# Performance work log

Hardware: AMD Instinct MI355X
Metric: run time of the kernel (lower is better)

## Reference

```python
import jax, jax.numpy as jnp
import numpy as np

N = 50000
H = 256
EPS = 1e-5

def setup_inputs() -> dict:
    key = jax.random.key(0)
    ks = jax.random.split(key, 8)
    d = 128
    inp = {
        'x': jax.random.normal(ks[0], (N, d), jnp.float32),
        'edge_index': jax.random.randint(ks[1], (2, 800000), 0, N, jnp.int64),
        'W1': jax.random.normal(ks[2], (d, H), jnp.float32) * (2.0 / d) ** 0.5,
        'b1': jnp.zeros((H,), jnp.float32),
        'g1': jnp.ones((H,), jnp.float32),
        'be1': jnp.zeros((H,), jnp.float32),
        'W2': jax.random.normal(ks[3], (H, H), jnp.float32) * (2.0 / H) ** 0.5,
        'b2': jnp.zeros((H,), jnp.float32),
        'g2': jnp.ones((H,), jnp.float32),
        'be2': jnp.zeros((H,), jnp.float32),
        'W3': jax.random.normal(ks[4], (H, H), jnp.float32) * (2.0 / H) ** 0.5,
        'b3': jnp.zeros((H,), jnp.float32),
        'g3': jnp.ones((H,), jnp.float32),
        'be3': jnp.zeros((H,), jnp.float32),
        'Wf1': jax.random.normal(ks[5], (H, H // 2), jnp.float32) * (2.0 / H) ** 0.5,
        'bf1': jnp.zeros((H // 2,), jnp.float32),
        'Wf2': jax.random.normal(ks[6], (H // 2, 1), jnp.float32) * (2.0 / (H // 2)) ** 0.5,
        'bf2': jnp.zeros((1,), jnp.float32),
    }
    return inp

def _gcn_norm(edge_index):
    # add self-loops, symmetric normalization (PyG GCNConv defaults)
    loop = jnp.arange(N, dtype=edge_index.dtype)
    row = jnp.concatenate([edge_index[0], loop])  # source
    col = jnp.concatenate([edge_index[1], loop])  # target
    deg = jax.ops.segment_sum(jnp.ones_like(col, jnp.float32), col, num_segments=N)
    dis = jnp.where(deg > 0, jax.lax.rsqrt(deg), 0.0)
    norm = dis[row] * dis[col]  # [E+N]
    return row, col, norm

def _conv(x, W, b, row, col, norm):
    xw = x @ W                       # [N,H]
    msg = xw[row] * norm[:, None]    # gather + scale, [E+N,H]
    out = jax.ops.segment_sum(msg, col, num_segments=N)
    return out + b

def _ln(x, g, b):
    mu = jnp.mean(x, axis=-1, keepdims=True)
    var = jnp.var(x, axis=-1, keepdims=True)
    return (x - mu) * jax.lax.rsqrt(var + EPS) * g + b

def reference(x, edge_index, W1, b1, g1, be1, W2, b2, g2, be2, W3, b3, g3, be3, Wf1, bf1, Wf2, bf2):
    row, col, norm = _gcn_norm(edge_index)
    x1 = jax.nn.relu(_ln(_conv(x, W1, b1, row, col, norm), g1, be1))
    x2 = jax.nn.relu(_ln(_conv(x1, W2, b2, row, col, norm), g2, be2)) + 0.7 * x1
    x3 = jax.nn.relu(_ln(_conv(x2, W3, b3, row, col, norm), g3, be3)) * 0.7 + x2
    h = jax.nn.relu(x3 @ Wf1 + bf1)
    return h @ Wf2 + bf2  # [N,1]
```

## Files before the change

kernel.cpp:

```cpp
#include <hip/hip_runtime.h>
#include <cstdint>
#include <cstddef>

#define HDIM 256
#define DIN 128
#define EPSV 1e-5f
#define SCHUNK 1024

typedef __attribute__((ext_vector_type(8))) short short8;
typedef __attribute__((ext_vector_type(4))) float f32x4;

__device__ __forceinline__ float bf2f(unsigned int u16) {
  union { unsigned int i; float f; } v; v.i = u16 << 16; return v.f;
}
__device__ __forceinline__ unsigned short f2bf(float f) {
  union { float f; unsigned int i; } v; v.f = f;
  unsigned int u = v.i;
  return (unsigned short)((u + 0x7fffu + ((u >> 16) & 1u)) >> 16);
}
__device__ __forceinline__ float4 ldbf4(const unsigned short* p) {
  uint2 v = *(const uint2*)p;
  return make_float4(bf2f(v.x & 0xffffu), bf2f(v.x >> 16),
                     bf2f(v.y & 0xffffu), bf2f(v.y >> 16));
}
__device__ __forceinline__ void stbf4(unsigned short* p, float a, float b, float c, float d) {
  uint2 o;
  o.x = (unsigned int)f2bf(a) | ((unsigned int)f2bf(b) << 16);
  o.y = (unsigned int)f2bf(c) | ((unsigned int)f2bf(d) << 16);
  *(uint2*)p = o;
}

__global__ __launch_bounds__(256) void zero_i_k(int* deg, int* cur, int n) {
  int i = blockIdx.x * 256 + threadIdx.x;
  if (i < n) { deg[i] = 0; cur[i] = 0; }
}

__global__ __launch_bounds__(256) void hist_k(const int* __restrict__ col, int* deg, int e) {
  int i = blockIdx.x * 256 + threadIdx.x;
  if (i < e) atomicAdd(&deg[col[i]], 1);
}

__global__ __launch_bounds__(256) void scanA_k(const int* __restrict__ deg,
                                               int* __restrict__ row_ptr,
                                               int* __restrict__ blockSums,
                                               float* __restrict__ dis, int n) {
  __shared__ int waveSums[4];
  const int tid = threadIdx.x, lane = tid & 63, w = tid >> 6;
  const int base = blockIdx.x * SCHUNK + tid * 4;
  int v0 = 0, v1 = 0, v2 = 0, v3 = 0;
  if (base + 0 < n) v0 = deg[base + 0];
  if (base + 1 < n) v1 = deg[base + 1];
  if (base + 2 < n) v2 = deg[base + 2];
  if (base + 3 < n) v3 = deg[base + 3];
  if (base + 0 < n) dis[base + 0] = rsqrtf((float)(v0 + 1));
  if (base + 1 < n) dis[base + 1] = rsqrtf((float)(v1 + 1));
  if (base + 2 < n) dis[base + 2] = rsqrtf((float)(v2 + 1));
  if (base + 3 < n) dis[base + 3] = rsqrtf((float)(v3 + 1));
  int tsum = v0 + v1 + v2 + v3;
  int inc = tsum;
#pragma unroll
  for (int off = 1; off < 64; off <<= 1) {
    int t = __shfl_up(inc, off);
    if (lane >= off) inc += t;
  }
  if (lane == 63) waveSums[w] = inc;
  __syncthreads();
  int woff = 0;
#pragma unroll
  for (int k = 0; k < 4; ++k) woff += (k < w) ? waveSums[k] : 0;
  int excl = woff + inc - tsum;
  if (base + 0 < n) row_ptr[base + 0] = excl;
  if (base + 1 < n) row_ptr[base + 1] = excl + v0;
  if (base + 2 < n) row_ptr[base + 2] = excl + v0 + v1;
  if (base + 3 < n) row_ptr[base + 3] = excl + v0 + v1 + v2;
  if (tid == 255) blockSums[blockIdx.x] = woff + inc;
}

__global__ __launch_bounds__(256) void scanB_k(int* blockSums, int nb) {
  __shared__ int waveSums[4];
  const int tid = threadIdx.x, lane = tid & 63, w = tid >> 6;
  int v = (tid < nb) ? blockSums[tid] : 0;
  int inc = v;
#pragma unroll
  for (int off = 1; off < 64; off <<= 1) {
    int t = __shfl_up(inc, off);
    if (lane >= off) inc += t;
  }
  if (lane == 63) waveSums[w] = inc;
  __syncthreads();
  int woff = 0;
#pragma unroll
  for (int k = 0; k < 4; ++k) woff += (k < w) ? waveSums[k] : 0;
  if (tid < nb) blockSums[tid] = woff + inc - v;
}

__global__ __launch_bounds__(256) void scanC_k(int* __restrict__ row_ptr,
                                               const int* __restrict__ blockSums,
                                               int n, int e) {
  const int base = blockIdx.x * SCHUNK + threadIdx.x * 4;
  const int add = blockSums[blockIdx.x];
#pragma unroll
  for (int k = 0; k < 4; ++k)
    if (base + k < n) row_ptr[base + k] += add;
  if (blockIdx.x == 0 && threadIdx.x == 0) row_ptr[n] = e;
}

__global__ __launch_bounds__(256) void fill_k(const int* __restrict__ row,
                                              const int* __restrict__ col,
                                              const int* __restrict__ row_ptr,
                                              int* cur, int* srcs, int e) {
  int i = blockIdx.x * 256 + threadIdx.x;
  if (i < e) {
    int c = col[i];
    int p = row_ptr[c] + atomicAdd(&cur[c], 1);
    srcs[p] = row[i];
  }
}

__device__ __forceinline__ void packW(const float* __restrict__ W,
                                      unsigned short* __restrict__ out,
                                      int idx, int C) {
  int j = idx & 7, lane = (idx >> 3) & 63, rest = idx >> 9;
  int NSUB = C >> 4;
  int ns = rest % NSUB, kb = rest / NSUB;
  int k = kb * 32 + (lane >> 4) * 8 + j;
  int c = ns * 16 + (lane & 15);
  out[idx] = f2bf(W[(size_t)k * C + c]);
}

__global__ __launch_bounds__(256) void prep_k(
    const float* __restrict__ W1, const float* __restrict__ W2,
    const float* __restrict__ W3, const float* __restrict__ Wf1,
    const float* __restrict__ x,
    unsigned short* __restrict__ W1p, unsigned short* __restrict__ W2p,
    unsigned short* __restrict__ W3p, unsigned short* __restrict__ Wf1p,
    unsigned short* __restrict__ xbf, int nx) {
  int idx = blockIdx.x * 256 + threadIdx.x;
  const int s0 = DIN * HDIM, s1 = s0 + HDIM * HDIM, s2 = s1 + HDIM * HDIM,
            s3 = s2 + HDIM * 128;
  if (idx < s0) packW(W1, W1p, idx, HDIM);
  else if (idx < s1) packW(W2, W2p, idx - s0, HDIM);
  else if (idx < s2) packW(W3, W3p, idx - s1, HDIM);
  else if (idx < s3) packW(Wf1, Wf1p, idx - s2, 128);
  else if (idx - s3 < nx) xbf[idx - s3] = f2bf(x[idx - s3]);
}

__global__ __launch_bounds__(256) void gather256_k(
    const unsigned short* __restrict__ x, const int* __restrict__ row_ptr,
    const int* __restrict__ srcs, const float* __restrict__ dis,
    unsigned short* __restrict__ out, int n) {
  int i = blockIdx.x * 4 + (threadIdx.x >> 6);
  int lane = threadIdx.x & 63;
  if (i >= n) return;
  int beg = row_ptr[i], end = row_ptr[i + 1];
  const int co = lane * 4;
  float di = dis[i];
  float4 sv = ldbf4(x + (size_t)i * 256 + co);
  float4 acc = make_float4(di * sv.x, di * sv.y, di * sv.z, di * sv.w);
  int j = beg;
  for (; j + 8 <= end; j += 8) {
    int r0 = srcs[j], r1 = srcs[j + 1], r2 = srcs[j + 2], r3 = srcs[j + 3];
    int r4 = srcs[j + 4], r5 = srcs[j + 5], r6 = srcs[j + 6], r7 = srcs[j + 7];
    float d0 = dis[r0], d1 = dis[r1], d2 = dis[r2], d3 = dis[r3];
    float d4 = dis[r4], d5 = dis[r5], d6 = dis[r6], d7 = dis[r7];
    float4 v0 = ldbf4(x + (size_t)r0 * 256 + co);
    float4 v1 = ldbf4(x + (size_t)r1 * 256 + co);
    float4 v2 = ldbf4(x + (size_t)r2 * 256 + co);
    float4 v3 = ldbf4(x + (size_t)r3 * 256 + co);
    float4 v4 = ldbf4(x + (size_t)r4 * 256 + co);
    float4 v5 = ldbf4(x + (size_t)r5 * 256 + co);
    float4 v6 = ldbf4(x + (size_t)r6 * 256 + co);
    float4 v7 = ldbf4(x + (size_t)r7 * 256 + co);
    acc.x += ((d0*v0.x + d1*v1.x) + (d2*v2.x + d3*v3.x)) + ((d4*v4.x + d5*v5.x) + (d6*v6.x + d7*v7.x));
    acc.y += ((d0*v0.y + d1*v1.y) + (d2*v2.y + d3*v3.y)) + ((d4*v4.y + d5*v5.y) + (d6*v6.y + d7*v7.y));
    acc.z += ((d0*v0.z + d1*v1.z) + (d2*v2.z + d3*v3.z)) + ((d4*v4.z + d5*v5.z) + (d6*v6.z + d7*v7.z));
    acc.w += ((d0*v0.w + d1*v1.w) + (d2*v2.w + d3*v3.w)) + ((d4*v4.w + d5*v5.w) + (d6*v6.w + d7*v7.w));
  }
  for (; j < end; ++j) {
    int r = srcs[j];
    float d = dis[r];
    float4 v = ldbf4(x + (size_t)r * 256 + co);
    acc.x += d * v.x; acc.y += d * v.y; acc.z += d * v.z; acc.w += d * v.w;
  }
  stbf4(out + (size_t)i * 256 + co, di * acc.x, di * acc.y, di * acc.z, di * acc.w);
}

__global__ __launch_bounds__(256) void gather128_k(
    const unsigned short* __restrict__ x, const int* __restrict__ row_ptr,
    const int* __restrict__ srcs, const float* __restrict__ dis,
    unsigned short* __restrict__ out, int n) {
  int i = blockIdx.x * 4 + (threadIdx.x >> 6);
  int lane = threadIdx.x & 63;
  if (i >= n) return;
  int beg = row_ptr[i], end = row_ptr[i + 1];
  const int co = lane * 2;
  float di = dis[i];
  unsigned int sv = *(const unsigned int*)(x + (size_t)i * 128 + co);
  float ax = di * bf2f(sv & 0xffffu), ay = di * bf2f(sv >> 16);
  int j = beg;
  for (; j + 8 <= end; j += 8) {
    int r0 = srcs[j], r1 = srcs[j + 1], r2 = srcs[j + 2], r3 = srcs[j + 3];
    int r4 = srcs[j + 4], r5 = srcs[j + 5], r6 = srcs[j + 6], r7 = srcs[j + 7];
    float d0 = dis[r0], d1 = dis[r1], d2 = dis[r2], d3 = dis[r3];
    float d4 = dis[r4], d5 = dis[r5], d6 = dis[r6], d7 = dis[r7];
    unsigned int u0 = *(const unsigned int*)(x + (size_t)r0 * 128 + co);
    unsigned int u1 = *(const unsigned int*)(x + (size_t)r1 * 128 + co);
    unsigned int u2 = *(const unsigned int*)(x + (size_t)r2 * 128 + co);
    unsigned int u3 = *(const unsigned int*)(x + (size_t)r3 * 128 + co);
    unsigned int u4 = *(const unsigned int*)(x + (size_t)r4 * 128 + co);
    unsigned int u5 = *(const unsigned int*)(x + (size_t)r5 * 128 + co);
    unsigned int u6 = *(const unsigned int*)(x + (size_t)r6 * 128 + co);
    unsigned int u7 = *(const unsigned int*)(x + (size_t)r7 * 128 + co);
    ax += ((d0*bf2f(u0&0xffffu) + d1*bf2f(u1&0xffffu)) + (d2*bf2f(u2&0xffffu) + d3*bf2f(u3&0xffffu)))
        + ((d4*bf2f(u4&0xffffu) + d5*bf2f(u5&0xffffu)) + (d6*bf2f(u6&0xffffu) + d7*bf2f(u7&0xffffu)));
    ay += ((d0*bf2f(u0>>16) + d1*bf2f(u1>>16)) + (d2*bf2f(u2>>16) + d3*bf2f(u3>>16)))
        + ((d4*bf2f(u4>>16) + d5*bf2f(u5>>16)) + (d6*bf2f(u6>>16) + d7*bf2f(u7>>16)));
  }
  for (; j < end; ++j) {
    int r = srcs[j];
    float d = dis[r];
    unsigned int u = *(const unsigned int*)(x + (size_t)r * 128 + co);
    ax += d * bf2f(u & 0xffffu);
    ay += d * bf2f(u >> 16);
  }
  unsigned int o = (unsigned int)f2bf(di * ax) | ((unsigned int)f2bf(di * ay) << 16);
  *(unsigned int*)(out + (size_t)i * 128 + co) = o;
}

template<int MODE, int K>
__global__ __launch_bounds__(512) void gemmln_k(
    const unsigned short* __restrict__ A, const unsigned short* __restrict__ Wp,
    const float* __restrict__ bias, const float* __restrict__ gam,
    const float* __restrict__ bet, const unsigned short* __restrict__ xprev,
    unsigned short* __restrict__ out, int n) {
  constexpr int CN = 256, NSUB = 16, KC = K / 32;
  __shared__ float red_s[64][4], red_q[64][4];
  const int t = threadIdx.x;
  const int w = t >> 6, lane = t & 63;
  const int rg = w & 1, cg = w >> 1;
  const int gq = lane >> 4, i = lane & 15;
  const int m0 = blockIdx.x * 64;
  const int r0 = m0 + rg * 32 + i, r1 = r0 + 16;
  const int l0 = r0 < n ? r0 : n - 1, l1 = r1 < n ? r1 : n - 1;
  const unsigned short* a0 = A + (size_t)l0 * K + gq * 8;
  const unsigned short* a1 = A + (size_t)l1 * K + gq * 8;
  const short8* wp = (const short8*)Wp + (size_t)(cg * 4) * 64 + lane;

  f32x4 acc[2][4];
#pragma unroll
  for (int rr = 0; rr < 2; ++rr)
#pragma unroll
    for (int j = 0; j < 4; ++j) acc[rr][j] = (f32x4){0.f, 0.f, 0.f, 0.f};

  short8 af0 = *(const short8*)a0;
  short8 af1 = *(const short8*)a1;
  short8 wf[4];
#pragma unroll
  for (int j = 0; j < 4; ++j) wf[j] = wp[j * 64];

#pragma unroll
  for (int kc = 0; kc < KC; ++kc) {
    short8 naf0, naf1, nwf[4];
    if (kc + 1 < KC) {
      naf0 = *(const short8*)(a0 + (kc + 1) * 32);
      naf1 = *(const short8*)(a1 + (kc + 1) * 32);
#pragma unroll
      for (int j = 0; j < 4; ++j) nwf[j] = wp[(size_t)(kc + 1) * NSUB * 64 + j * 64];
    }
#pragma unroll
    for (int j = 0; j < 4; ++j) {
      acc[0][j] = __builtin_amdgcn_mfma_f32_16x16x32_bf16(wf[j], af0, acc[0][j], 0, 0, 0);
      acc[1][j] = __builtin_amdgcn_mfma_f32_16x16x32_bf16(wf[j], af1, acc[1][j], 0, 0, 0);
    }
    if (kc + 1 < KC) {
      af0 = naf0; af1 = naf1;
#pragma unroll
      for (int j = 0; j < 4; ++j) wf[j] = nwf[j];
    }
  }

  const int colb = cg * 64 + gq * 4;
  float s0 = 0.f, q0 = 0.f, s1 = 0.f, q1 = 0.f;
#pragma unroll
  for (int j = 0; j < 4; ++j) {
    f32x4 b4 = *(const f32x4*)(bias + colb + j * 16);
#pragma unroll
    for (int r = 0; r < 4; ++r) {
      acc[0][j][r] += b4[r];
      acc[1][j][r] += b4[r];
      float v = acc[0][j][r]; s0 += v; q0 += v * v;
      float u = acc[1][j][r]; s1 += u; q1 += u * u;
    }
  }
  s0 += __shfl_xor(s0, 16); s0 += __shfl_xor(s0, 32);
  q0 += __shfl_xor(q0, 16); q0 += __shfl_xor(q0, 32);
  s1 += __shfl_xor(s1, 16); s1 += __shfl_xor(s1, 32);
  q1 += __shfl_xor(q1, 16); q1 += __shfl_xor(q1, 32);
  if (gq == 0) {
    red_s[rg * 32 + i][cg] = s0;      red_q[rg * 32 + i][cg] = q0;
    red_s[rg * 32 + 16 + i][cg] = s1; red_q[rg * 32 + 16 + i][cg] = q1;
  }
  __syncthreads();

#pragma unroll
  for (int rr = 0; rr < 2; ++rr) {
    int il = rg * 32 + rr * 16 + i;
    int r = m0 + il;
    if (r >= n) continue;
    float ss = (red_s[il][0] + red_s[il][1]) + (red_s[il][2] + red_s[il][3]);
    float qq = (red_q[il][0] + red_q[il][1]) + (red_q[il][2] + red_q[il][3]);
    float mu = ss * (1.f / CN);
    float inv = rsqrtf(qq * (1.f / CN) - mu * mu + EPSV);
    unsigned short* op = out + (size_t)r * CN + colb;
    const unsigned short* pp = (MODE != 0) ? (xprev + (size_t)r * CN + colb) : nullptr;
#pragma unroll
    for (int j = 0; j < 4; ++j) {
      f32x4 g4 = *(const f32x4*)(gam + colb + j * 16);
      f32x4 e4 = *(const f32x4*)(bet + colb + j * 16);
      float o0 = fmaxf((acc[rr][j][0] - mu) * inv * g4[0] + e4[0], 0.f);
      float o1 = fmaxf((acc[rr][j][1] - mu) * inv * g4[1] + e4[1], 0.f);
      float o2 = fmaxf((acc[rr][j][2] - mu) * inv * g4[2] + e4[2], 0.f);
      float o3 = fmaxf((acc[rr][j][3] - mu) * inv * g4[3] + e4[3], 0.f);
      if (MODE == 1) {
        float4 pv = ldbf4(pp + j * 16);
        o0 += 0.7f * pv.x; o1 += 0.7f * pv.y; o2 += 0.7f * pv.z; o3 += 0.7f * pv.w;
      } else if (MODE == 2) {
        float4 pv = ldbf4(pp + j * 16);
        o0 = o0 * 0.7f + pv.x; o1 = o1 * 0.7f + pv.y;
        o2 = o2 * 0.7f + pv.z; o3 = o3 * 0.7f + pv.w;
      }
      stbf4(op + j * 16, o0, o1, o2, o3);
    }
  }
}

__global__ __launch_bounds__(256) void gemmdot_k(
    const unsigned short* __restrict__ A, const unsigned short* __restrict__ Wp,
    const float* __restrict__ b1, const float* __restrict__ w2,
    const float* __restrict__ b2, float* __restrict__ out, int n) {
  constexpr int K = 256, NSUB = 8, KC = 8;
  __shared__ float redh[64][2];
  const int t = threadIdx.x;
  const int w = t >> 6, lane = t & 63;
  const int rg = w & 1, cg = w >> 1;
  const int gq = lane >> 4, i = lane & 15;
  const int m0 = blockIdx.x * 64;
  const int r0 = m0 + rg * 32 + i, r1 = r0 + 16;
  const int l0 = r0 < n ? r0 : n - 1, l1 = r1 < n ? r1 : n - 1;
  const unsigned short* a0 = A + (size_t)l0 * K + gq * 8;
  const unsigned short* a1 = A + (size_t)l1 * K + gq * 8;
  const short8* wp = (const short8*)Wp + (size_t)(cg * 4) * 64 + lane;

  f32x4 acc[2][4];
#pragma unroll
  for (int rr = 0; rr < 2; ++rr)
#pragma unroll
    for (int j = 0; j < 4; ++j) acc[rr][j] = (f32x4){0.f, 0.f, 0.f, 0.f};

  short8 af0 = *(const short8*)a0;
  short8 af1 = *(const short8*)a1;
  short8 wf[4];
#pragma unroll
  for (int j = 0; j < 4; ++j) wf[j] = wp[j * 64];

#pragma unroll
  for (int kc = 0; kc < KC; ++kc) {
    short8 naf0, naf1, nwf[4];
    if (kc + 1 < KC) {
      naf0 = *(const short8*)(a0 + (kc + 1) * 32);
      naf1 = *(const short8*)(a1 + (kc + 1) * 32);
#pragma unroll
      for (int j = 0; j < 4; ++j) nwf[j] = wp[(size_t)(kc + 1) * NSUB * 64 + j * 64];
    }
#pragma unroll
    for (int j = 0; j < 4; ++j) {
      acc[0][j] = __builtin_amdgcn_mfma_f32_16x16x32_bf16(wf[j], af0, acc[0][j], 0, 0, 0);
      acc[1][j] = __builtin_amdgcn_mfma_f32_16x16x32_bf16(wf[j], af1, acc[1][j], 0, 0, 0);
    }
    if (kc + 1 < KC) {
      af0 = naf0; af1 = naf1;
#pragma unroll
      for (int j = 0; j < 4; ++j) wf[j] = nwf[j];
    }
  }

  const int colb = cg * 64 + gq * 4;
  float p0 = 0.f, p1 = 0.f;
#pragma unroll
  for (int j = 0; j < 4; ++j) {
    f32x4 bb = *(const f32x4*)(b1 + colb + j * 16);
    f32x4 ww = *(const f32x4*)(w2 + colb + j * 16);
#pragma unroll
    for (int r = 0; r < 4; ++r) {
      p0 += fmaxf(acc[0][j][r] + bb[r], 0.f) * ww[r];
      p1 += fmaxf(acc[1][j][r] + bb[r], 0.f) * ww[r];
    }
  }
  p0 += __shfl_xor(p0, 16); p0 += __shfl_xor(p0, 32);
  p1 += __shfl_xor(p1, 16); p1 += __shfl_xor(p1, 32);
  if (gq == 0) {
    redh[rg * 32 + i][cg] = p0;
    redh[rg * 32 + 16 + i][cg] = p1;
  }
  __syncthreads();
  if (t < 64) {
    int r = m0 + t;
    if (r < n) out[r] = redh[t][0] + redh[t][1] + b2[0];
  }
}

extern "C" void kernel_launch(void* const* d_in, const int* in_sizes, int n_in,
                              void* d_out, int out_size, void* d_ws, size_t ws_size,
                              hipStream_t stream) {
  const float* x   = (const float*)d_in[0];
  const int*   ei  = (const int*)d_in[1];
  const float* W1  = (const float*)d_in[2];
  const float* b1  = (const float*)d_in[3];
  const float* g1  = (const float*)d_in[4];
  const float* be1 = (const float*)d_in[5];
  const float* W2  = (const float*)d_in[6];
  const float* b2  = (const float*)d_in[7];
  const float* g2  = (const float*)d_in[8];
  const float* be2 = (const float*)d_in[9];
  const float* W3  = (const float*)d_in[10];
  const float* b3  = (const float*)d_in[11];
  const float* g3  = (const float*)d_in[12];
  const float* be3 = (const float*)d_in[13];
  const float* Wf1 = (const float*)d_in[14];
  const float* bf1 = (const float*)d_in[15];
  const float* Wf2 = (const float*)d_in[16];
  const float* bf2 = (const float*)d_in[17];
  float* out = (float*)d_out;

  const int n = in_sizes[0] / DIN;
  const int e = in_sizes[1] / 2;
  const int* row = ei;
  const int* col = ei + e;

  char* ws = (char*)d_ws;
  size_t off = 0;
  auto alloc = [&](size_t bytes) -> void* {
    void* p = ws + off;
    off = (off + bytes + 255) & ~(size_t)255;
    return p;
  };
  float*          dis     = (float*)alloc((size_t)n * 4);
  int*            deg_i   = (int*)alloc((size_t)n * 4);
  int*            cur     = (int*)alloc((size_t)n * 4);
  int*            row_ptr = (int*)alloc((size_t)(n + 1) * 4);
  int*            bsums   = (int*)alloc((size_t)256 * 4);
  int*            srcs    = (int*)alloc((size_t)e * 4);
  unsigned short* W1p     = (unsigned short*)alloc((size_t)DIN * HDIM * 2);
  unsigned short* W2p     = (unsigned short*)alloc((size_t)HDIM * HDIM * 2);
  unsigned short* W3p     = (unsigned short*)alloc((size_t)HDIM * HDIM * 2);
  unsigned short* Wf1p    = (unsigned short*)alloc((size_t)HDIM * 128 * 2);
  unsigned short* xbf     = (unsigned short*)alloc((size_t)n * DIN * 2);
  unsigned short* agg     = (unsigned short*)alloc((size_t)n * HDIM * 2);
  unsigned short* x1      = (unsigned short*)alloc((size_t)n * HDIM * 2);
  unsigned short* x2      = (unsigned short*)alloc((size_t)n * HDIM * 2);
  unsigned short* a1      = agg;
  unsigned short* x3      = x1;

  const int nb  = (n + 255) / 256;
  const int eb  = (e + 255) / 256;
  const int lnb = (n + 3) / 4;
  const int gb  = (n + 63) / 64;
  const int sb_ = (n + SCHUNK - 1) / SCHUNK;
  const int prep_tot = DIN * HDIM + HDIM * HDIM + HDIM * HDIM + HDIM * 128 + n * DIN;

  zero_i_k<<<nb, 256, 0, stream>>>(deg_i, cur, n);
  hist_k<<<eb, 256, 0, stream>>>(col, deg_i, e);
  scanA_k<<<sb_, 256, 0, stream>>>(deg_i, row_ptr, bsums, dis, n);
  scanB_k<<<1, 256, 0, stream>>>(bsums, sb_);
  scanC_k<<<sb_, 256, 0, stream>>>(row_ptr, bsums, n, e);
  fill_k<<<eb, 256, 0, stream>>>(row, col, row_ptr, cur, srcs, e);

  prep_k<<<(prep_tot + 255) / 256, 256, 0, stream>>>(W1, W2, W3, Wf1, x,
                                                     W1p, W2p, W3p, Wf1p, xbf, n * DIN);

  gather128_k<<<lnb, 256, 0, stream>>>(xbf, row_ptr, srcs, dis, a1, n);
  gemmln_k<0, DIN><<<gb, 512, 0, stream>>>(a1, W1p, b1, g1, be1, nullptr, x1, n);

  gather256_k<<<lnb, 256, 0, stream>>>(x1, row_ptr, srcs, dis, agg, n);
  gemmln_k<1, HDIM><<<gb, 512, 0, stream>>>(agg, W2p, b2, g2, be2, x1, x2, n);

  gather256_k<<<lnb, 256, 0, stream>>>(x2, row_ptr, srcs, dis, agg, n);
  gemmln_k<2, HDIM><<<gb, 512, 0, stream>>>(agg, W3p, b3, g3, be3, x2, x3, n);

  gemmdot_k<<<gb, 256, 0, stream>>>(x3, Wf1p, bf1, Wf2, bf2, out, n);
}
```

Measured before the change: 470.6 us.

## Prescale gather sources by inverse sqrt degree and widen gather loads to 16 bytes

```diff
diff --git a/kernel.cpp b/kernel.cpp
--- a/kernel.cpp
+++ b/kernel.cpp
@@ -29,6 +29,11 @@
   o.y = (unsigned int)f2bf(c) | ((unsigned int)f2bf(d) << 16);
   *(uint2*)p = o;
 }
+#define ACC8(u) do { \
+    acc[0] += bf2f((u).x & 0xffffu); acc[1] += bf2f((u).x >> 16); \
+    acc[2] += bf2f((u).y & 0xffffu); acc[3] += bf2f((u).y >> 16); \
+    acc[4] += bf2f((u).z & 0xffffu); acc[5] += bf2f((u).z >> 16); \
+    acc[6] += bf2f((u).w & 0xffffu); acc[7] += bf2f((u).w >> 16); } while (0)
 
 __global__ __launch_bounds__(256) void zero_i_k(int* deg, int* cur, int n) {
   int i = blockIdx.x * 256 + threadIdx.x;
@@ -131,10 +136,10 @@
 __global__ __launch_bounds__(256) void prep_k(
     const float* __restrict__ W1, const float* __restrict__ W2,
     const float* __restrict__ W3, const float* __restrict__ Wf1,
-    const float* __restrict__ x,
+    const float* __restrict__ x, const float* __restrict__ dis,
     unsigned short* __restrict__ W1p, unsigned short* __restrict__ W2p,
     unsigned short* __restrict__ W3p, unsigned short* __restrict__ Wf1p,
-    unsigned short* __restrict__ xbf, int nx) {
+    unsigned short* __restrict__ xs, int nx) {
   int idx = blockIdx.x * 256 + threadIdx.x;
   const int s0 = DIN * HDIM, s1 = s0 + HDIM * HDIM, s2 = s1 + HDIM * HDIM,
             s3 = s2 + HDIM * 128;
@@ -142,89 +147,118 @@
   else if (idx < s1) packW(W2, W2p, idx - s0, HDIM);
   else if (idx < s2) packW(W3, W3p, idx - s1, HDIM);
   else if (idx < s3) packW(Wf1, Wf1p, idx - s2, 128);
-  else if (idx - s3 < nx) xbf[idx - s3] = f2bf(x[idx - s3]);
+  else {
+    int o = idx - s3;
+    if (o < nx) xs[o] = f2bf(x[o] * dis[o >> 7]);
+  }
 }
 
 __global__ __launch_bounds__(256) void gather256_k(
-    const unsigned short* __restrict__ x, const int* __restrict__ row_ptr,
+    const unsigned short* __restrict__ xs, const int* __restrict__ row_ptr,
     const int* __restrict__ srcs, const float* __restrict__ dis,
     unsigned short* __restrict__ out, int n) {
-  int i = blockIdx.x * 4 + (threadIdx.x >> 6);
+  int wv = blockIdx.x * 4 + (threadIdx.x >> 6);
   int lane = threadIdx.x & 63;
-  if (i >= n) return;
-  int beg = row_ptr[i], end = row_ptr[i + 1];
-  const int co = lane * 4;
-  float di = dis[i];
-  float4 sv = ldbf4(x + (size_t)i * 256 + co);
-  float4 acc = make_float4(di * sv.x, di * sv.y, di * sv.z, di * sv.w);
+  int half = lane >> 5, li = lane & 31;
+  int i = wv * 2 + half;
+  bool valid = i < n;
+  int ic = valid ? i : n - 1;
+  int beg = row_ptr[ic], end = row_ptr[ic + 1];
+  float di = dis[ic];
+  const int co = li * 8;
+  const unsigned short* xb = xs + co;
+  float acc[8];
+  {
+    uint4 v = *(const uint4*)(xb + (size_t)ic * 256);
+    acc[0] = bf2f(v.x & 0xffffu); acc[1] = bf2f(v.x >> 16);
+    acc[2] = bf2f(v.y & 0xffffu); acc[3] = bf2f(v.y >> 16);
+    acc[4] = bf2f(v.z & 0xffffu); acc[5] = bf2f(v.z >> 16);
+    acc[6] = bf2f(v.w & 0xffffu); acc[7] = bf2f(v.w >> 16);
+  }
   int j = beg;
-  for (; j + 8 <= end; j += 8) {
-    int r0 = srcs[j], r1 = srcs[j + 1], r2 = srcs[j + 2], r3 = srcs[j + 3];
-    int r4 = srcs[j + 4], r5 = srcs[j + 5], r6 = srcs[j + 6], r7 = srcs[j + 7];
-    float d0 = dis[r0], d1 = dis[r1], d2 = dis[r2], d3 = dis[r3];
-    float d4 = dis[r4], d5 = dis[r5], d6 = dis[r6], d7 = dis[r7];
-    float4 v0 = ldbf4(x + (size_t)r0 * 256 + co);
-    float4 v1 = ldbf4(x + (size_t)r1 * 256 + co);
-    float4 v2 = ldbf4(x + (size_t)r2 * 256 + co);
-    float4 v3 = ldbf4(x + (size_t)r3 * 256 + co);
-    float4 v4 = ldbf4(x + (size_t)r4 * 256 + co);
-    float4 v5 = ldbf4(x + (size_t)r5 * 256 + co);
-    float4 v6 = ldbf4(x + (size_t)r6 * 256 + co);
-    float4 v7 = ldbf4(x + (size_t)r7 * 256 + co);
-    acc.x += ((d0*v0.x + d1*v1.x) + (d2*v2.x + d3*v3.x)) + ((d4*v4.x + d5*v5.x) + (d6*v6.x + d7*v7.x));
-    acc.y += ((d0*v0.y + d1*v1.y) + (d2*v2.y + d3*v3.y)) + ((d4*v4.y + d5*v5.y) + (d6*v6.y + d7*v7.y));
-    acc.z += ((d0*v0.z + d1*v1.z) + (d2*v2.z + d3*v3.z)) + ((d4*v4.z + d5*v5.z) + (d6*v6.z + d7*v7.z));
-    acc.w += ((d0*v0.w + d1*v1.w) + (d2*v2.w + d3*v3.w)) + ((d4*v4.w + d5*v5.w) + (d6*v6.w + d7*v7.w));
+  int4 sA, sB;
+  if (j + 8 <= end) { sA = *(const int4*)(srcs + j); sB = *(const int4*)(srcs + j + 4); }
+  for (; j + 8 <= end;) {
+    int4 cA = sA, cB = sB;
+    j += 8;
+    if (j + 8 <= end) { sA = *(const int4*)(srcs + j); sB = *(const int4*)(srcs + j + 4); }
+    uint4 u0 = *(const uint4*)(xb + (size_t)cA.x * 256);
+    uint4 u1 = *(const uint4*)(xb + (size_t)cA.y * 256);
+    uint4 u2 = *(const uint4*)(xb + (size_t)cA.z * 256);
+    uint4 u3 = *(const uint4*)(xb + (size_t)cA.w * 256);
+    uint4 u4 = *(const uint4*)(xb + (size_t)cB.x * 256);
+    uint4 u5 = *(const uint4*)(xb + (size_t)cB.y * 256);
+    uint4 u6 = *(const uint4*)(xb + (size_t)cB.z * 256);
+    uint4 u7 = *(const uint4*)(xb + (size_t)cB.w * 256);
+    ACC8(u0); ACC8(u1); ACC8(u2); ACC8(u3);
+    ACC8(u4); ACC8(u5); ACC8(u6); ACC8(u7);
   }
   for (; j < end; ++j) {
-    int r = srcs[j];
-    float d = dis[r];
-    float4 v = ldbf4(x + (size_t)r * 256 + co);
-    acc.x += d * v.x; acc.y += d * v.y; acc.z += d * v.z; acc.w += d * v.w;
-  }
-  stbf4(out + (size_t)i * 256 + co, di * acc.x, di * acc.y, di * acc.z, di * acc.w);
+    uint4 u = *(const uint4*)(xb + (size_t)srcs[j] * 256);
+    ACC8(u);
+  }
+  if (valid) {
+    uint4 o;
+    o.x = (unsigned int)f2bf(di * acc[0]) | ((unsigned int)f2bf(di * acc[1]) << 16);
+    o.y = (unsigned int)f2bf(di * acc[2]) | ((unsigned int)f2bf(di * acc[3]) << 16);
+    o.z = (unsigned int)f2bf(di * acc[4]) | ((unsigned int)f2bf(di * acc[5]) << 16);
+    o.w = (unsigned int)f2bf(di * acc[6]) | ((unsigned int)f2bf(di * acc[7]) << 16);
+    *(uint4*)(out + (size_t)i * 256 + co) = o;
+  }
 }
 
 __global__ __launch_bounds__(256) void gather128_k(
-    const unsigned short* __restrict__ x, const int* __restrict__ row_ptr,
+    const unsigned short* __restrict__ xs, const int* __restrict__ row_ptr,
     const int* __restrict__ srcs, const float* __restrict__ dis,
     unsigned short* __restrict__ out, int n) {
-  int i = blockIdx.x * 4 + (threadIdx.x >> 6);
+  int wv = blockIdx.x * 4 + (threadIdx.x >> 6);
   int lane = threadIdx.x & 63;
-  if (i >= n) return;
-  int beg = row_ptr[i], end = row_ptr[i + 1];
-  const int co = lane * 2;
-  float di = dis[i];
-  unsigned int sv = *(const unsigned int*)(x + (size_t)i * 128 + co);
-  float ax = di * bf2f(sv & 0xffffu), ay = di * bf2f(sv >> 16);
+  int q = lane >> 4, li = lane & 15;
+  int i = wv * 4 + q;
+  bool valid = i < n;
+  int ic = valid ? i : n - 1;
+  int beg = row_ptr[ic], end = row_ptr[ic + 1];
+  float di = dis[ic];
+  const int co = li * 8;
+  const unsigned short* xb = xs + co;
+  float acc[8];
+  {
+    uint4 v = *(const uint4*)(xb + (size_t)ic * 128);
+    acc[0] = bf2f(v.x & 0xffffu); acc[1] = bf2f(v.x >> 16);
+    acc[2] = bf2f(v.y & 0xffffu); acc[3] = bf2f(v.y >> 16);
+    acc[4] = bf2f(v.z & 0xffffu); acc[5] = bf2f(v.z >> 16);
+    acc[6] = bf2f(v.w & 0xffffu); acc[7] = bf2f(v.w >> 16);
+  }
   int j = beg;
-  for (; j + 8 <= end; j += 8) {
-    int r0 = srcs[j], r1 = srcs[j + 1], r2 = srcs[j + 2], r3 = srcs[j + 3];
-    int r4 = srcs[j + 4], r5 = srcs[j + 5], r6 = srcs[j + 6], r7 = srcs[j + 7];
-    float d0 = dis[r0], d1 = dis[r1], d2 = dis[r2], d3 = dis[r3];
-    float d4 = dis[r4], d5 = dis[r5], d6 = dis[r6], d7 = dis[r7];
-    unsigned int u0 = *(const unsigned int*)(x + (size_t)r0 * 128 + co);
-    unsigned int u1 = *(const unsigned int*)(x + (size_t)r1 * 128 + co);
-    unsigned int u2 = *(const unsigned int*)(x + (size_t)r2 * 128 + co);
-    unsigned int u3 = *(const unsigned int*)(x + (size_t)r3 * 128 + co);
-    unsigned int u4 = *(const unsigned int*)(x + (size_t)r4 * 128 + co);
-    unsigned int u5 = *(const unsigned int*)(x + (size_t)r5 * 128 + co);
-    unsigned int u6 = *(const unsigned int*)(x + (size_t)r6 * 128 + co);
-    unsigned int u7 = *(const unsigned int*)(x + (size_t)r7 * 128 + co);
-    ax += ((d0*bf2f(u0&0xffffu) + d1*bf2f(u1&0xffffu)) + (d2*bf2f(u2&0xffffu) + d3*bf2f(u3&0xffffu)))
-        + ((d4*bf2f(u4&0xffffu) + d5*bf2f(u5&0xffffu)) + (d6*bf2f(u6&0xffffu) + d7*bf2f(u7&0xffffu)));
-    ay += ((d0*bf2f(u0>>16) + d1*bf2f(u1>>16)) + (d2*bf2f(u2>>16) + d3*bf2f(u3>>16)))
-        + ((d4*bf2f(u4>>16) + d5*bf2f(u5>>16)) + (d6*bf2f(u6>>16) + d7*bf2f(u7>>16)));
+  int4 sA, sB;
+  if (j + 8 <= end) { sA = *(const int4*)(srcs + j); sB = *(const int4*)(srcs + j + 4); }
+  for (; j + 8 <= end;) {
+    int4 cA = sA, cB = sB;
+    j += 8;
+    if (j + 8 <= end) { sA = *(const int4*)(srcs + j); sB = *(const int4*)(srcs + j + 4); }
+    uint4 u0 = *(const uint4*)(xb + (size_t)cA.x * 128);
+    uint4 u1 = *(const uint4*)(xb + (size_t)cA.y * 128);
+    uint4 u2 = *(const uint4*)(xb + (size_t)cA.z * 128);
+    uint4 u3 = *(const uint4*)(xb + (size_t)cA.w * 128);
+    uint4 u4 = *(const uint4*)(xb + (size_t)cB.x * 128);
+    uint4 u5 = *(const uint4*)(xb + (size_t)cB.y * 128);
+    uint4 u6 = *(const uint4*)(xb + (size_t)cB.z * 128);
+    uint4 u7 = *(const uint4*)(xb + (size_t)cB.w * 128);
+    ACC8(u0); ACC8(u1); ACC8(u2); ACC8(u3);
+    ACC8(u4); ACC8(u5); ACC8(u6); ACC8(u7);
   }
   for (; j < end; ++j) {
-    int r = srcs[j];
-    float d = dis[r];
-    unsigned int u = *(const unsigned int*)(x + (size_t)r * 128 + co);
-    ax += d * bf2f(u & 0xffffu);
-    ay += d * bf2f(u >> 16);
-  }
-  unsigned int o = (unsigned int)f2bf(di * ax) | ((unsigned int)f2bf(di * ay) << 16);
-  *(unsigned int*)(out + (size_t)i * 128 + co) = o;
+    uint4 u = *(const uint4*)(xb + (size_t)srcs[j] * 128);
+    ACC8(u);
+  }
+  if (valid) {
+    uint4 o;
+    o.x = (unsigned int)f2bf(di * acc[0]) | ((unsigned int)f2bf(di * acc[1]) << 16);
+    o.y = (unsigned int)f2bf(di * acc[2]) | ((unsigned int)f2bf(di * acc[3]) << 16);
+    o.z = (unsigned int)f2bf(di * acc[4]) | ((unsigned int)f2bf(di * acc[5]) << 16);
+    o.w = (unsigned int)f2bf(di * acc[6]) | ((unsigned int)f2bf(di * acc[7]) << 16);
+    *(uint4*)(out + (size_t)i * 128 + co) = o;
+  }
 }
 
 template<int MODE, int K>
@@ -232,7 +266,8 @@
     const unsigned short* __restrict__ A, const unsigned short* __restrict__ Wp,
     const float* __restrict__ bias, const float* __restrict__ gam,
     const float* __restrict__ bet, const unsigned short* __restrict__ xprev,
-    unsigned short* __restrict__ out, int n) {
+    const float* __restrict__ dis, unsigned short* __restrict__ out,
+    unsigned short* __restrict__ outs, int n) {
   constexpr int CN = 256, NSUB = 16, KC = K / 32;
   __shared__ float red_s[64][4], red_q[64][4];
   const int t = threadIdx.x;
@@ -311,7 +346,9 @@
     float qq = (red_q[il][0] + red_q[il][1]) + (red_q[il][2] + red_q[il][3]);
     float mu = ss * (1.f / CN);
     float inv = rsqrtf(qq * (1.f / CN) - mu * mu + EPSV);
+    float sdi = outs ? dis[r] : 0.f;
     unsigned short* op = out + (size_t)r * CN + colb;
+    unsigned short* osp = outs ? outs + (size_t)r * CN + colb : nullptr;
     const unsigned short* pp = (MODE != 0) ? (xprev + (size_t)r * CN + colb) : nullptr;
 #pragma unroll
     for (int j = 0; j < 4; ++j) {
@@ -330,6 +367,7 @@
         o2 = o2 * 0.7f + pv.z; o3 = o3 * 0.7f + pv.w;
       }
       stbf4(op + j * 16, o0, o1, o2, o3);
+      if (outs) stbf4(osp + j * 16, o0 * sdi, o1 * sdi, o2 * sdi, o3 * sdi);
     }
   }
 }
@@ -454,18 +492,21 @@
   unsigned short* W2p     = (unsigned short*)alloc((size_t)HDIM * HDIM * 2);
   unsigned short* W3p     = (unsigned short*)alloc((size_t)HDIM * HDIM * 2);
   unsigned short* Wf1p    = (unsigned short*)alloc((size_t)HDIM * 128 * 2);
-  unsigned short* xbf     = (unsigned short*)alloc((size_t)n * DIN * 2);
+  unsigned short* xsb     = (unsigned short*)alloc((size_t)n * DIN * 2);
   unsigned short* agg     = (unsigned short*)alloc((size_t)n * HDIM * 2);
   unsigned short* x1      = (unsigned short*)alloc((size_t)n * HDIM * 2);
+  unsigned short* x1s     = (unsigned short*)alloc((size_t)n * HDIM * 2);
   unsigned short* x2      = (unsigned short*)alloc((size_t)n * HDIM * 2);
+  unsigned short* x2s     = (unsigned short*)alloc((size_t)n * HDIM * 2);
   unsigned short* a1      = agg;
   unsigned short* x3      = x1;
 
   const int nb  = (n + 255) / 256;
   const int eb  = (e + 255) / 256;
-  const int lnb = (n + 3) / 4;
   const int gb  = (n + 63) / 64;
   const int sb_ = (n + SCHUNK - 1) / SCHUNK;
+  const int g2b = (n + 7) / 8;
+  const int g1b = (n + 15) / 16;
   const int prep_tot = DIN * HDIM + HDIM * HDIM + HDIM * HDIM + HDIM * 128 + n * DIN;
 
   zero_i_k<<<nb, 256, 0, stream>>>(deg_i, cur, n);
@@ -475,17 +516,17 @@
   scanC_k<<<sb_, 256, 0, stream>>>(row_ptr, bsums, n, e);
   fill_k<<<eb, 256, 0, stream>>>(row, col, row_ptr, cur, srcs, e);
 
-  prep_k<<<(prep_tot + 255) / 256, 256, 0, stream>>>(W1, W2, W3, Wf1, x,
-                                                     W1p, W2p, W3p, Wf1p, xbf, n * DIN);
-
-  gather128_k<<<lnb, 256, 0, stream>>>(xbf, row_ptr, srcs, dis, a1, n);
-  gemmln_k<0, DIN><<<gb, 512, 0, stream>>>(a1, W1p, b1, g1, be1, nullptr, x1, n);
-
-  gather256_k<<<lnb, 256, 0, stream>>>(x1, row_ptr, srcs, dis, agg, n);
-  gemmln_k<1, HDIM><<<gb, 512, 0, stream>>>(agg, W2p, b2, g2, be2, x1, x2, n);
-
-  gather256_k<<<lnb, 256, 0, stream>>>(x2, row_ptr, srcs, dis, agg, n);
-  gemmln_k<2, HDIM><<<gb, 512, 0, stream>>>(agg, W3p, b3, g3, be3, x2, x3, n);
+  prep_k<<<(prep_tot + 255) / 256, 256, 0, stream>>>(W1, W2, W3, Wf1, x, dis,
+                                                     W1p, W2p, W3p, Wf1p, xsb, n * DIN);
+
+  gather128_k<<<g1b, 256, 0, stream>>>(xsb, row_ptr, srcs, dis, a1, n);
+  gemmln_k<0, DIN><<<gb, 512, 0, stream>>>(a1, W1p, b1, g1, be1, nullptr, dis, x1, x1s, n);
+
+  gather256_k<<<g2b, 256, 0, stream>>>(x1s, row_ptr, srcs, dis, agg, n);
+  gemmln_k<1, HDIM><<<gb, 512, 0, stream>>>(agg, W2p, b2, g2, be2, x1, dis, x2, x2s, n);
+
+  gather256_k<<<g2b, 256, 0, stream>>>(x2s, row_ptr, srcs, dis, agg, n);
+  gemmln_k<2, HDIM><<<gb, 512, 0, stream>>>(agg, W3p, b3, g3, be3, x2, dis, x3, nullptr, n);
 
   gemmdot_k<<<gb, 256, 0, stream>>>(x3, Wf1p, bf1, Wf2, bf2, out, n);
 }
```

New measurement: 484.6 us. 3.0% more time.
